# Kernel optimization log

Measured on AMD Instinct MI355X. Metric: run time of the kernel, lower is better.

## Reference

```python
import jax, jax.numpy as jnp
import numpy as np

# dims
BS = 4096
MOVE = 4
N_EN, ED = 64, 16
N_AL, AD = 63, 16
OTHER = 20
MF = MOVE + OTHER            # m_f_size = 24
IN = MOVE + N_EN * ED + N_AL * AD + OTHER  # 2056
H = 4                        # n_head
HE = 128                     # hypernet_emb
E = 64                       # attention_dim (emb_dim)
NA = N_EN + N_AL + 1         # n_agents = 128
RNN = 256
EN_START = MOVE
AL_START = MOVE + N_EN * ED
OTH_START = AL_START + N_AL * AD


def setup_inputs() -> dict:
    key = jax.random.key(0)
    ks = jax.random.split(key, 32)
    g = lambda k, shape: (jax.random.normal(k, shape, dtype=jnp.float32) * 0.05)
    return {
        "obs": jax.random.normal(ks[0], (BS, IN), dtype=jnp.float32),
        # per-head query MLP (Linear(MF,HE)+ReLU+Linear(HE,E,no bias)), stacked over heads
        "Wq1": g(ks[1], (H, HE, MF)), "bq1": g(ks[2], (H, HE)), "Wq2": g(ks[3], (H, E, HE)),
        # per-head key_m MLP
        "Wkm1": g(ks[4], (H, HE, MF)), "bkm1": g(ks[5], (H, HE)), "Wkm2": g(ks[6], (H, E, HE)),
        # per-head entity key linears (no bias)
        "Wke": g(ks[7], (H, E, ED)), "Wka": g(ks[8], (H, E, AD)),
        # per-head value_m MLP
        "Wvm1": g(ks[9], (H, HE, MF)), "bvm1": g(ks[10], (H, HE)), "Wvm2": g(ks[11], (H, E, HE)),
        # per-head entity value linears (no bias)
        "Wve": g(ks[12], (H, E, ED)), "Wva": g(ks[13], (H, E, AD)),
        # b net: Linear(IN,E)+ReLU+Linear(E,1)
        "Wb1": g(ks[14], (E, IN)), "bb1": g(ks[15], (E,)), "Wb2": g(ks[16], (1, E)), "bb2": g(ks[17], (1,)),
        # hyper_w_head: Linear(IN,HE)+ReLU+Linear(HE,H)
        "Wh1": g(ks[18], (HE, IN)), "bh1": g(ks[19], (HE,)), "Wh2": g(ks[20], (H, HE)), "bh2": g(ks[21], (H,)),
        # final layer: Linear(E*NA, RNN)
        "Wf": g(ks[22], (RNN, E * NA)), "bf": g(ks[23], (RNN,)),
    }


def _headed_mlp(x, W1, b1, W2):
    # x: [B, MF]; W1: [H, HE, MF]; W2: [H, E, HE] -> [B, H, E]
    h = jax.nn.relu(jnp.einsum("bf,hgf->bhg", x, W1) + b1[None])
    return jnp.einsum("bhg,heg->bhe", h, W2)


def reference(obs, Wq1, bq1, Wq2, Wkm1, bkm1, Wkm2, Wke, Wka,
              Wvm1, bvm1, Wvm2, Wve, Wva, Wb1, bb1, Wb2, bb2,
              Wh1, bh1, Wh2, bh2, Wf, bf):
    bs = obs.shape[0]
    m = jnp.concatenate([obs[:, :MOVE], obs[:, OTH_START:]], axis=1)        # [B, MF]
    enemies = obs[:, EN_START:AL_START].reshape(bs, N_EN, ED)               # [B, N_EN, ED]
    allies = obs[:, AL_START:OTH_START].reshape(bs, N_AL, AD)               # [B, N_AL, AD]

    q = _headed_mlp(m, Wq1, bq1, Wq2)                                       # [B, H, E]
    km = _headed_mlp(m, Wkm1, bkm1, Wkm2)[:, :, None, :]                    # [B, H, 1, E]
    ke = jnp.einsum("bnd,hed->bhne", enemies, Wke)                          # [B, H, N_EN, E]
    ka = jnp.einsum("bnd,hed->bhne", allies, Wka)                           # [B, H, N_AL, E]
    k = jnp.concatenate([km, ke, ka], axis=2)                               # [B, H, NA, E]

    vm = _headed_mlp(m, Wvm1, bvm1, Wvm2)[:, :, None, :]
    ve = jnp.einsum("bnd,hed->bhne", enemies, Wve)
    va = jnp.einsum("bnd,hed->bhne", allies, Wva)
    v = jnp.concatenate([vm, ve, va], axis=2)                               # [B, H, NA, E]

    logits = jnp.einsum("bhe,bhne->bhn", q, k) / np.sqrt(E).astype(np.float32)
    w = jax.nn.softmax(logits, axis=-1)                                     # [B, H, NA]
    # torch: atten_w (B,1,NA) expanded to (B,E,NA) * v permuted to (B,E,NA); flatten [E,NA]
    scores = (w[:, :, None, :] * jnp.swapaxes(v, 2, 3)).reshape(bs, H, E * NA)

    b_term = jax.nn.relu(obs @ Wb1.T + bb1) @ Wb2.T + bb2                   # [B, 1]
    w_head = jnp.abs(jax.nn.relu(obs @ Wh1.T + bh1) @ Wh2.T + bh2)          # [B, H]
    mixed = jnp.einsum("bhk,bh->bk", scores, w_head) + b_term               # [B, E*NA]
    return mixed @ Wf.T + bf                                                # [B, RNN]
```

## Files before the change

kernel.cpp:

```cpp
#include <hip/hip_runtime.h>
#include <hip/hip_bf16.h>

typedef __attribute__((ext_vector_type(8))) short short8;
typedef __attribute__((ext_vector_type(4))) float floatx4;

#define NIN 2056
#define KPAD 2080
#define NBS 4096

__device__ __forceinline__ void gl_lds16(const ushort* g, ushort* l) {
#if defined(__has_builtin) && __has_builtin(__builtin_amdgcn_global_load_lds)
  __builtin_amdgcn_global_load_lds(
      (const __attribute__((address_space(1))) unsigned int*)g,
      (__attribute__((address_space(3))) unsigned int*)l, 16, 0, 0);
#else
  *(uint4*)l = *(const uint4*)g;
#endif
}

__device__ __forceinline__ float wsum(float v) {
#pragma unroll
  for (int o = 32; o; o >>= 1) v += __shfl_xor(v, o, 64);
  return v;
}
__device__ __forceinline__ float wmax(float v) {
#pragma unroll
  for (int o = 32; o; o >>= 1) v = fmaxf(v, __shfl_xor(v, o, 64));
  return v;
}

__global__ void prep_small(const float* __restrict__ obs,
                           const float* __restrict__ Wb1, const float* __restrict__ Wh1,
                           const float* __restrict__ Wq1, const float* __restrict__ Wkm1,
                           const float* __restrict__ Wvm1, const float* __restrict__ bq1,
                           const float* __restrict__ bkm1, const float* __restrict__ bvm1,
                           const float* __restrict__ Wq2, const float* __restrict__ Wkm2,
                           const float* __restrict__ Wvm2,
                           const float* __restrict__ Wke, const float* __restrict__ Wka,
                           __hip_bfloat16* __restrict__ mmat,
                           __hip_bfloat16* __restrict__ w1cat,
                           __hip_bfloat16* __restrict__ w1m, float* __restrict__ b1cat,
                           __hip_bfloat16* __restrict__ w2cat,
                           __hip_bfloat16* __restrict__ wket,
                           __hip_bfloat16* __restrict__ wkat) {
  int bid = blockIdx.x, tid = threadIdx.x;
  if (bid < 512) {
    int idx = bid * 256 + tid;
    int b = idx >> 5, j = idx & 31;
    float v = 0.f;
    if (j < 4) v = obs[(size_t)b * NIN + j];
    else if (j < 24) v = obs[(size_t)b * NIN + 2032 + j];
    mmat[idx] = __float2bfloat16(v);
  } else if (bid < 704) {
    int r = bid - 512;
    const float* src = (r < 64) ? (Wb1 + (size_t)r * NIN) : (Wh1 + (size_t)(r - 64) * NIN);
    for (int j = tid; j < KPAD; j += 256)
      w1cat[(size_t)r * KPAD + j] = __float2bfloat16(j < NIN ? src[j] : 0.f);
  } else if (bid < 896) {
    int idx = (bid - 704) * 256 + tid;
    int row = idx >> 5, j = idx & 31;
    int net = row >> 9, hg = row & 511;
    const float* W1 = net == 0 ? Wq1 : (net == 1 ? Wkm1 : Wvm1);
    float v = (j < 24) ? W1[(size_t)hg * 24 + j] : 0.f;
    w1m[idx] = __float2bfloat16(v);
    if (j == 0) {
      const float* b1 = net == 0 ? bq1 : (net == 1 ? bkm1 : bvm1);
      b1cat[row] = b1[hg];
    }
  } else if (bid < 1280) {
    int idx = (bid - 896) * 256 + tid;
    int row = idx >> 7, g = idx & 127;
    int net = row >> 8, he = row & 255;
    const float* W2 = net == 0 ? Wq2 : (net == 1 ? Wkm2 : Wvm2);
    w2cat[idx] = __float2bfloat16(W2[(size_t)he * 128 + g]);
  } else {
    const float* W = (bid == 1280) ? Wke : Wka;
    __hip_bfloat16* dst = (bid == 1280) ? wket : wkat;
    for (int j = tid; j < 4096; j += 256) {
      int e = j & 63, hd = j >> 6;
      int h = hd >> 4, d = hd & 15;
      dst[j] = __float2bfloat16(W[h * 1024 + e * 16 + d]);
    }
  }
}

__global__ void p6a_twf(const float* __restrict__ Wf, float* __restrict__ Wft,
                        float* __restrict__ rowsum) {
  __shared__ float t[64][65];
  int kt = blockIdx.x, rt = blockIdx.y;
  int tid = threadIdx.x;
  int kl = tid & 63, r0 = tid >> 6;
#pragma unroll
  for (int ii = 0; ii < 16; ++ii) {
    int rl = ii * 4 + r0;
    t[rl][kl] = Wf[(size_t)(rt * 64 + rl) * 8192 + kt * 64 + kl];
  }
  __syncthreads();
#pragma unroll
  for (int ii = 0; ii < 16; ++ii) {
    int kl2 = ii * 4 + r0;
    Wft[(size_t)(kt * 64 + kl2) * 256 + rt * 64 + kl] = t[kl][kl2];
  }
  if (tid < 64) {
    float s = 0.f;
    for (int kk = 0; kk < 64; ++kk) s += t[tid][kk];
    atomicAdd(&rowsum[rt * 64 + tid], s);
  }
}

__global__ void p6b_yt(const float* __restrict__ Wft, const float* __restrict__ Wve,
                       const float* __restrict__ Wva, __hip_bfloat16* __restrict__ Yt) {
  int n = blockIdx.x;
  int r = threadIdx.x;
  if (n == 0) {
    alignas(16) __hip_bfloat16 tmp[8];
    for (int e0 = 0; e0 < 64; e0 += 8) {
#pragma unroll
      for (int j = 0; j < 8; ++j)
        tmp[j] = __float2bfloat16(Wft[(size_t)((e0 + j) * 128) * 256 + r]);
      *(uint4*)(Yt + (size_t)r * 8192 + (e0 >> 4) * 2048 + 2032 + (e0 & 15)) =
          *(const uint4*)tmp;
    }
    return;
  }
  const float* Wv = (n <= 64) ? Wve : Wva;
  float accv[64];
#pragma unroll
  for (int j = 0; j < 64; ++j) accv[j] = 0.f;
  for (int e = 0; e < 64; ++e) {
    float v = Wft[(size_t)(e * 128 + n) * 256 + r];
#pragma unroll
    for (int hd = 0; hd < 64; ++hd)
      accv[hd] += Wv[(hd >> 4) * 1024 + e * 16 + (hd & 15)] * v;
  }
#pragma unroll
  for (int c = 0; c < 8; ++c) {
    alignas(16) __hip_bfloat16 tmp[8];
#pragma unroll
    for (int j = 0; j < 8; ++j) tmp[j] = __float2bfloat16(accv[c * 8 + j]);
    *(uint4*)(Yt + (size_t)r * 8192 + (c >> 1) * 2048 + (size_t)(n - 1) * 16 + (c & 1) * 8) =
        *(const uint4*)tmp;
  }
}

__global__ __launch_bounds__(256) void qkv_fused(
    const __hip_bfloat16* __restrict__ mmat_, const __hip_bfloat16* __restrict__ w1m_,
    const float* __restrict__ b1cat, const __hip_bfloat16* __restrict__ w2cat_,
    const __hip_bfloat16* __restrict__ wket_, const __hip_bfloat16* __restrict__ wkat_,
    float* __restrict__ QKV, float* __restrict__ QKE, float* __restrict__ QKA) {
  __shared__ alignas(16) ushort lH[64 * 136];
  __shared__ alignas(16) ushort lq[64 * 72];
  const ushort* mmat = (const ushort*)mmat_;
  const ushort* w1m = (const ushort*)w1m_;
  const ushort* w2cat = (const ushort*)w2cat_;
  const ushort* wket = (const ushort*)wket_;
  const ushort* wkat = (const ushort*)wkat_;
  int mt = blockIdx.x, z = blockIdx.y;
  int t = threadIdx.x;
  int w = t >> 6, l = t & 63, r16 = l & 15, kg = l >> 4;
  floatx4 zero4 = {0.f, 0.f, 0.f, 0.f};
  short8 a1 = *(const short8*)(mmat + (size_t)(mt * 64 + w * 16 + r16) * 32 + kg * 8);
  floatx4 acc1[8];
#pragma unroll
  for (int c = 0; c < 8; ++c) {
    short8 b1 = *(const short8*)(w1m + (size_t)(z * 128 + c * 16 + r16) * 32 + kg * 8);
    acc1[c] = __builtin_amdgcn_mfma_f32_16x16x32_bf16(a1, b1, zero4, 0, 0, 0);
  }
#pragma unroll
  for (int c = 0; c < 8; ++c) {
    int col = c * 16 + r16;
    float bias = b1cat[z * 128 + col];
#pragma unroll
    for (int r = 0; r < 4; ++r) {
      float v = acc1[c][r] + bias;
      v = v > 0.f ? v : 0.f;
      __hip_bfloat16 bv = __float2bfloat16(v);
      lH[(w * 16 + kg * 4 + r) * 136 + col] = *(ushort*)&bv;
    }
  }
  __syncthreads();
  floatx4 acc2[4] = {zero4, zero4, zero4, zero4};
#pragma unroll
  for (int ks = 0; ks < 4; ++ks) {
    short8 a = *(const short8*)(lH + (w * 16 + r16) * 136 + ks * 32 + kg * 8);
#pragma unroll
    for (int c = 0; c < 4; ++c) {
      short8 b = *(const short8*)(w2cat + (size_t)(z * 64 + c * 16 + r16) * 128 + ks * 32 + kg * 8);
      acc2[c] = __builtin_amdgcn_mfma_f32_16x16x32_bf16(a, b, acc2[c], 0, 0, 0);
    }
  }
  float* Q = QKV + (size_t)(mt * 64) * 768 + z * 64;
#pragma unroll
  for (int c = 0; c < 4; ++c)
#pragma unroll
    for (int r = 0; r < 4; ++r)
      Q[(size_t)(w * 16 + kg * 4 + r) * 768 + c * 16 + r16] = acc2[c][r];
  if (z < 4) {
#pragma unroll
    for (int c = 0; c < 4; ++c)
#pragma unroll
      for (int r = 0; r < 4; ++r) {
        __hip_bfloat16 bv = __float2bfloat16(acc2[c][r]);
        lq[(w * 16 + kg * 4 + r) * 72 + c * 16 + r16] = *(ushort*)&bv;
      }
    short8 a0 = *(const short8*)(lq + (w * 16 + r16) * 72 + kg * 8);
    short8 a1q = *(const short8*)(lq + (w * 16 + r16) * 72 + 32 + kg * 8);
    const ushort* bke = wket + (size_t)(z * 16 + r16) * 64 + kg * 8;
    const ushort* bka = wkat + (size_t)(z * 16 + r16) * 64 + kg * 8;
    short8 bk0 = *(const short8*)bke;
    short8 bk1 = *(const short8*)(bke + 32);
    short8 ba0 = *(const short8*)bka;
    short8 ba1 = *(const short8*)(bka + 32);
    floatx4 ke = __builtin_amdgcn_mfma_f32_16x16x32_bf16(a0, bk0, zero4, 0, 0, 0);
    ke = __builtin_amdgcn_mfma_f32_16x16x32_bf16(a1q, bk1, ke, 0, 0, 0);
    floatx4 ka = __builtin_amdgcn_mfma_f32_16x16x32_bf16(a0, ba0, zero4, 0, 0, 0);
    ka = __builtin_amdgcn_mfma_f32_16x16x32_bf16(a1q, ba1, ka, 0, 0, 0);
#pragma unroll
    for (int r = 0; r < 4; ++r) {
      size_t row = (size_t)(mt * 64 + w * 16 + kg * 4 + r);
      QKE[row * 64 + z * 16 + r16] = ke[r];
      QKA[row * 64 + z * 16 + r16] = ka[r];
    }
  }
}

__global__ __launch_bounds__(256) void gemm_h1(
    const float* __restrict__ obs, const __hip_bfloat16* __restrict__ w1cat_,
    float* __restrict__ H1p) {
  __shared__ alignas(16) ushort lA[64 * 40];
  __shared__ alignas(16) ushort lB[192 * 40];
  const ushort* w1cat = (const ushort*)w1cat_;
  int mt = blockIdx.x, z = blockIdx.y;
  int t = threadIdx.x;
  int w = t >> 6, l = t & 63, r16 = l & 15, kg = l >> 4;
  int srow = t >> 2, sc = (t & 3) * 8;
  int k0 = z * 256;
  const float* ga = obs + (size_t)(mt * 64 + srow) * NIN + k0 + sc;
  ushort* sa = lA + srow * 40 + sc;
  const ushort* fa = lA + (w * 16 + r16) * 40 + kg * 8;
  floatx4 zero4 = {0.f, 0.f, 0.f, 0.f};
  floatx4 acc[12];
#pragma unroll
  for (int c = 0; c < 12; ++c) acc[c] = zero4;
  int nK = (z == 7) ? 9 : 8;
  for (int ks = 0; ks < nK; ++ks) {
    float4 f0, f1;
    bool tail = (z == 7 && ks == 8);
    if (!tail || (t & 3) == 0) {
      f0 = *(const float4*)(ga + ks * 32);
      f1 = *(const float4*)(ga + ks * 32 + 4);
    } else {
      f0 = make_float4(0.f, 0.f, 0.f, 0.f);
      f1 = make_float4(0.f, 0.f, 0.f, 0.f);
    }
    uint4 vb[3];
#pragma unroll
    for (int i = 0; i < 3; ++i)
      vb[i] = *(const uint4*)(w1cat + (size_t)(i * 64 + srow) * KPAD + k0 + sc + ks * 32);
    __syncthreads();
    alignas(16) __hip_bfloat16 tmp[8];
    tmp[0] = __float2bfloat16(f0.x); tmp[1] = __float2bfloat16(f0.y);
    tmp[2] = __float2bfloat16(f0.z); tmp[3] = __float2bfloat16(f0.w);
    tmp[4] = __float2bfloat16(f1.x); tmp[5] = __float2bfloat16(f1.y);
    tmp[6] = __float2bfloat16(f1.z); tmp[7] = __float2bfloat16(f1.w);
    *(uint4*)sa = *(const uint4*)tmp;
#pragma unroll
    for (int i = 0; i < 3; ++i)
      *(uint4*)(lB + (i * 64 + srow) * 40 + sc) = vb[i];
    __syncthreads();
    short8 a = *(const short8*)fa;
#pragma unroll
    for (int c = 0; c < 12; ++c) {
      short8 bb = *(const short8*)(lB + (c * 16 + r16) * 40 + kg * 8);
      acc[c] = __builtin_amdgcn_mfma_f32_16x16x32_bf16(a, bb, acc[c], 0, 0, 0);
    }
  }
  float* C = H1p + (size_t)z * NBS * 192;
  int row0 = mt * 64 + w * 16 + kg * 4;
#pragma unroll
  for (int c = 0; c < 12; ++c)
#pragma unroll
    for (int r = 0; r < 4; ++r)
      C[(size_t)(row0 + r) * 192 + c * 16 + r16] = acc[c][r];
}

__global__ __launch_bounds__(256) void gemm_final(
    const ushort* __restrict__ Xg, const ushort* __restrict__ Yt,
    float* __restrict__ part) {
  __shared__ alignas(16) ushort lA[128 * 32];
  __shared__ alignas(16) ushort lB[128 * 32];
  int bid = blockIdx.x;
  int z = bid & 7, nt = (bid >> 3) & 1, mt = bid >> 4;
  int t = threadIdx.x;
  int w = t >> 6, l = t & 63, r16 = l & 15, kg = l >> 4;
  int wr = (w >> 1) * 64, wc = (w & 1) * 64;
  const ushort* ga0 = Xg + (size_t)(mt * 128 + (t >> 2)) * 8192 + z * 1024 + (t & 3) * 8;
  const ushort* ga1 = ga0 + (size_t)64 * 8192;
  const ushort* gb0 = Yt + (size_t)(nt * 128 + (t >> 2)) * 8192 + z * 1024 + (t & 3) * 8;
  const ushort* gb1 = gb0 + (size_t)64 * 8192;
  ushort* la0 = lA + t * 8;
  ushort* la1 = lA + 2048 + t * 8;
  ushort* lb0 = lB + t * 8;
  ushort* lb1 = lB + 2048 + t * 8;
  const ushort* fa0 = lA + (wr + r16) * 32 + kg * 8;
  const ushort* fb0 = lB + (wc + r16) * 32 + kg * 8;
  floatx4 zero4 = {0.f, 0.f, 0.f, 0.f};
  floatx4 acc[4][4];
#pragma unroll
  for (int i = 0; i < 4; ++i)
#pragma unroll
    for (int j = 0; j < 4; ++j) acc[i][j] = zero4;
  for (int ks = 0; ks < 32; ++ks) {
    gl_lds16(ga0, la0);
    gl_lds16(ga1, la1);
    gl_lds16(gb0, lb0);
    gl_lds16(gb1, lb1);
    ga0 += 32; ga1 += 32; gb0 += 32; gb1 += 32;
    __syncthreads();
    short8 a[4], b[4];
#pragma unroll
    for (int mi = 0; mi < 4; ++mi) a[mi] = *(const short8*)(fa0 + mi * 512);
#pragma unroll
    for (int ni = 0; ni < 4; ++ni) b[ni] = *(const short8*)(fb0 + ni * 512);
#pragma unroll
    for (int mi = 0; mi < 4; ++mi)
#pragma unroll
      for (int ni = 0; ni < 4; ++ni)
        acc[mi][ni] = __builtin_amdgcn_mfma_f32_16x16x32_bf16(a[mi], b[ni], acc[mi][ni], 0, 0, 0);
    __syncthreads();
  }
  int row0 = mt * 128 + wr + kg * 4;
  int col0 = nt * 128 + wc + r16;
  float* cp = part + (size_t)z * NBS * 256;
#pragma unroll
  for (int mi = 0; mi < 4; ++mi)
#pragma unroll
    for (int ni = 0; ni < 4; ++ni)
#pragma unroll
      for (int r = 0; r < 4; ++r)
        cp[(size_t)(row0 + mi * 16 + r) * 256 + col0 + ni * 16] = acc[mi][ni][r];
}

__global__ __launch_bounds__(256) void row_kernel(
    const float* __restrict__ obs, const float* __restrict__ QKV,
    const float* __restrict__ QKE, const float* __restrict__ QKA,
    const float* __restrict__ H1p, const float* __restrict__ Wb2,
    const float* __restrict__ bb2, const float* __restrict__ Wh2,
    const float* __restrict__ bh2, const float* __restrict__ bb1,
    const float* __restrict__ bh1, __hip_bfloat16* __restrict__ X,
    float* __restrict__ bterm) {
  __shared__ float qke_lds[4][64], qka_lds[4][64];
  __shared__ uint4 xstage[4][2][256];
  int wv = threadIdx.x >> 6;
  int lane = threadIdx.x & 63;
  int b = blockIdx.x * 4 + wv;
  qke_lds[wv][lane] = QKE[(size_t)b * 64 + lane];
  qka_lds[wv][lane] = QKA[(size_t)b * 64 + lane];
  const float* qkv = QKV + (size_t)b * 768;
  float q_h[4], km_h[4], vm_h[4];
#pragma unroll
  for (int h = 0; h < 4; ++h) {
    q_h[h] = qkv[h * 64 + lane];
    km_h[h] = qkv[256 + h * 64 + lane];
    vm_h[h] = qkv[512 + h * 64 + lane];
  }
  float l0[4];
#pragma unroll
  for (int h = 0; h < 4; ++h) l0[h] = wsum(q_h[h] * km_h[h]) * 0.125f;
  const float* ob = obs + (size_t)b * NIN;
  alignas(16) float en[16];
  alignas(16) float al[16];
  {
    const float4* ep = (const float4*)(ob + 4 + lane * 16);
    const float4* ap = (const float4*)(ob + 1028 + lane * 16);
#pragma unroll
    for (int i = 0; i < 4; ++i) {
      *(float4*)(en + 4 * i) = ep[i];
      *(float4*)(al + 4 * i) = ap[i];
    }
  }
  bool av = lane < 63;
  float lE[4], lA_[4];
#pragma unroll
  for (int h = 0; h < 4; ++h) {
    float sE = 0.f, sA = 0.f;
#pragma unroll
    for (int d = 0; d < 16; ++d) {
      sE += en[d] * qke_lds[wv][h * 16 + d];
      sA += al[d] * qka_lds[wv][h * 16 + d];
    }
    lE[h] = sE * 0.125f;
    lA_[h] = sA * 0.125f;
  }
  float vb0 = 0.f, vw0 = 0.f, vw1 = 0.f;
  const size_t S1 = (size_t)NBS * 192;
#pragma unroll
  for (int z = 0; z < 8; ++z) {
    const float* p = H1p + (size_t)z * S1 + (size_t)b * 192;
    vb0 += p[lane];
    vw0 += p[64 + lane];
    vw1 += p[128 + lane];
  }
  float hb = fmaxf(vb0 + bb1[lane], 0.f);
  float bt = wsum(hb * Wb2[lane]) + bb2[0];
  float hw0 = fmaxf(vw0 + bh1[lane], 0.f);
  float hw1 = fmaxf(vw1 + bh1[64 + lane], 0.f);
  float whead[4];
#pragma unroll
  for (int h = 0; h < 4; ++h)
    whead[h] = fabsf(wsum(hw0 * Wh2[h * 128 + lane] + hw1 * Wh2[h * 128 + 64 + lane]) + bh2[h]);
  float wE[4], wA[4], w0[4];
#pragma unroll
  for (int h = 0; h < 4; ++h) {
    float mE = wmax(lE[h]);
    float mA = wmax(av ? lA_[h] : -3.0e38f);
    float mx = fmaxf(fmaxf(mE, mA), l0[h]);
    float pE = __expf(lE[h] - mx);
    float pA = av ? __expf(lA_[h] - mx) : 0.f;
    float p0 = __expf(l0[h] - mx);
    float den = wsum(pE + pA) + p0;
    float s = whead[h] / den;
    wE[h] = pE * s;
    wA[h] = pA * s;
    w0[h] = p0 * s;
  }
  __hip_bfloat16* xr = X + (size_t)b * 8192;
#pragma unroll
  for (int h = 0; h < 4; ++h) {
    int buf = h & 1;
    uint ue[8], ua[8];
#pragma unroll
    for (int j = 0; j < 8; ++j) {
      __hip_bfloat16 lo = __float2bfloat16(wE[h] * en[2 * j]);
      __hip_bfloat16 hi = __float2bfloat16(wE[h] * en[2 * j + 1]);
      ue[j] = (uint)*(ushort*)&lo | ((uint)*(ushort*)&hi << 16);
      __hip_bfloat16 alo = __float2bfloat16(wA[h] * al[2 * j]);
      __hip_bfloat16 ahi = __float2bfloat16(wA[h] * al[2 * j + 1]);
      ua[j] = (uint)*(ushort*)&alo | ((uint)*(ushort*)&ahi << 16);
    }
    xstage[wv][buf][lane * 2] = make_uint4(ue[0], ue[1], ue[2], ue[3]);
    xstage[wv][buf][lane * 2 + 1] = make_uint4(ue[4], ue[5], ue[6], ue[7]);
    if (av) {
      xstage[wv][buf][(64 + lane) * 2] = make_uint4(ua[0], ua[1], ua[2], ua[3]);
      xstage[wv][buf][(64 + lane) * 2 + 1] = make_uint4(ua[4], ua[5], ua[6], ua[7]);
    }
#pragma unroll
    for (int s = 0; s < 4; ++s) {
      uint4 v = xstage[wv][buf][s * 64 + lane];
      if (!(s == 3 && lane >= 62))
        *(uint4*)(xr + h * 2048 + s * 512 + lane * 8) = v;
    }
  }
  float x0 = w0[0] * vm_h[0] + w0[1] * vm_h[1] + w0[2] * vm_h[2] + w0[3] * vm_h[3];
  xr[(lane >> 4) * 2048 + 2032 + (lane & 15)] = __float2bfloat16(x0);
  if (lane == 0) bterm[b] = bt;
}

__global__ void k7_out(const float* __restrict__ part, const float* __restrict__ bterm,
                       const float* __restrict__ rowsum, const float* __restrict__ bfv,
                       float* __restrict__ out) {
  int b = blockIdx.x, r = threadIdx.x;
  size_t i = (size_t)b * 256 + r;
  const size_t S = (size_t)NBS * 256;
  float v = 0.f;
#pragma unroll
  for (int z = 0; z < 8; ++z) v += part[i + z * S];
  out[i] = v + bterm[b] * rowsum[r] + bfv[r];
}

extern "C" void kernel_launch(void* const* d_in, const int* in_sizes, int n_in,
                              void* d_out, int out_size, void* d_ws, size_t ws_size,
                              hipStream_t stream) {
  const float* obs = (const float*)d_in[0];
  const float* Wq1 = (const float*)d_in[1];
  const float* bq1 = (const float*)d_in[2];
  const float* Wq2 = (const float*)d_in[3];
  const float* Wkm1 = (const float*)d_in[4];
  const float* bkm1 = (const float*)d_in[5];
  const float* Wkm2 = (const float*)d_in[6];
  const float* Wke = (const float*)d_in[7];
  const float* Wka = (const float*)d_in[8];
  const float* Wvm1 = (const float*)d_in[9];
  const float* bvm1 = (const float*)d_in[10];
  const float* Wvm2 = (const float*)d_in[11];
  const float* Wve = (const float*)d_in[12];
  const float* Wva = (const float*)d_in[13];
  const float* Wb1 = (const float*)d_in[14];
  const float* bb1 = (const float*)d_in[15];
  const float* Wb2 = (const float*)d_in[16];
  const float* bb2 = (const float*)d_in[17];
  const float* Wh1 = (const float*)d_in[18];
  const float* bh1 = (const float*)d_in[19];
  const float* Wh2 = (const float*)d_in[20];
  const float* bh2 = (const float*)d_in[21];
  const float* Wf = (const float*)d_in[22];
  const float* bfv = (const float*)d_in[23];
  float* out = (float*)d_out;

  char* ws = (char*)d_ws;
  size_t off = 0;
  auto alloc = [&](size_t bytes) -> void* {
    void* p = ws + off;
    off += (bytes + 255) & ~(size_t)255;
    return p;
  };
  __hip_bfloat16* mmat = (__hip_bfloat16*)alloc((size_t)NBS * 32 * 2);
  __hip_bfloat16* w1m = (__hip_bfloat16*)alloc((size_t)1536 * 32 * 2);
  float* b1cat = (float*)alloc(1536 * 4);
  __hip_bfloat16* w2cat = (__hip_bfloat16*)alloc((size_t)768 * 128 * 2);
  __hip_bfloat16* w1cat = (__hip_bfloat16*)alloc((size_t)192 * KPAD * 2);
  __hip_bfloat16* wket = (__hip_bfloat16*)alloc(4096 * 2);
  __hip_bfloat16* wkat = (__hip_bfloat16*)alloc(4096 * 2);
  float* rowsum = (float*)alloc(256 * 4);
  float* bterm = (float*)alloc(NBS * 4);
  float* QKE = (float*)alloc((size_t)NBS * 64 * 4);
  float* QKA = (float*)alloc((size_t)NBS * 64 * 4);
  float* Wft = (float*)alloc((size_t)8192 * 256 * 4);
  __hip_bfloat16* Yt = (__hip_bfloat16*)alloc((size_t)256 * 8192 * 2);
  __hip_bfloat16* X = (__hip_bfloat16*)alloc((size_t)NBS * 8192 * 2);
  char* R = (char*)alloc((size_t)39 * 1024 * 1024);
  float* QKV = (float*)R;
  float* H1p = (float*)(R + (size_t)NBS * 768 * 4);
  float* part8 = (float*)R;

  hipMemsetAsync(rowsum, 0, 256 * 4, stream);

  prep_small<<<1282, 256, 0, stream>>>(obs, Wb1, Wh1, Wq1, Wkm1, Wvm1, bq1, bkm1, bvm1,
                                       Wq2, Wkm2, Wvm2, Wke, Wka,
                                       mmat, w1cat, w1m, b1cat, w2cat, wket, wkat);
  p6a_twf<<<dim3(128, 4), 256, 0, stream>>>(Wf, Wft, rowsum);
  p6b_yt<<<128, 256, 0, stream>>>(Wft, Wve, Wva, Yt);

  gemm_h1<<<dim3(64, 8), 256, 0, stream>>>(obs, w1cat, H1p);
  qkv_fused<<<dim3(64, 12), 256, 0, stream>>>(mmat, w1m, b1cat, w2cat, wket, wkat,
                                              QKV, QKE, QKA);
  row_kernel<<<NBS / 4, 256, 0, stream>>>(obs, QKV, QKE, QKA, H1p, Wb2, bb2, Wh2, bh2,
                                          bb1, bh1, X, bterm);
  gemm_final<<<512, 256, 0, stream>>>((const ushort*)X, (const ushort*)Yt, part8);
  k7_out<<<NBS, 256, 0, stream>>>(part8, bterm, rowsum, bfv, out);

  (void)in_sizes; (void)n_in; (void)out_size; (void)ws_size;
}
```

Before: 264.2 us.

## Split gemm_h1 over N tiles and prefetch next K-slice into registers

The gemm_h1 kernel now adds an N grid dimension (3 tiles of 64 columns), so each block computes a 64x64 output tile instead of 64x192. This triples the block count and cuts accumulator and LDS use per block. It also moves the global loads for the next K step after the barrier, so they overlap with the MFMA work on the current step. In exchange, each obs tile is read and converted three times.

```diff
diff --git a/kernel.cpp b/kernel.cpp
--- a/kernel.cpp
+++ b/kernel.cpp
@@ -228,60 +228,66 @@
     const float* __restrict__ obs, const __hip_bfloat16* __restrict__ w1cat_,
     float* __restrict__ H1p) {
   __shared__ alignas(16) ushort lA[64 * 40];
-  __shared__ alignas(16) ushort lB[192 * 40];
+  __shared__ alignas(16) ushort lB[64 * 40];
   const ushort* w1cat = (const ushort*)w1cat_;
-  int mt = blockIdx.x, z = blockIdx.y;
+  int mt = blockIdx.x, nt = blockIdx.y, z = blockIdx.z;
   int t = threadIdx.x;
   int w = t >> 6, l = t & 63, r16 = l & 15, kg = l >> 4;
   int srow = t >> 2, sc = (t & 3) * 8;
   int k0 = z * 256;
   const float* ga = obs + (size_t)(mt * 64 + srow) * NIN + k0 + sc;
+  const ushort* gb = w1cat + (size_t)(nt * 64 + srow) * KPAD + k0 + sc;
   ushort* sa = lA + srow * 40 + sc;
+  ushort* sb = lB + srow * 40 + sc;
   const ushort* fa = lA + (w * 16 + r16) * 40 + kg * 8;
+  const ushort* fb0 = lB + r16 * 40 + kg * 8;
   floatx4 zero4 = {0.f, 0.f, 0.f, 0.f};
-  floatx4 acc[12];
-#pragma unroll
-  for (int c = 0; c < 12; ++c) acc[c] = zero4;
+  floatx4 acc[4] = {zero4, zero4, zero4, zero4};
   int nK = (z == 7) ? 9 : 8;
+  bool aok = (t & 3) == 0;
+  float4 f0c, f1c;
+  uint4 vbc;
+  {
+    f0c = *(const float4*)(ga);
+    f1c = *(const float4*)(ga + 4);
+    vbc = *(const uint4*)(gb);
+  }
   for (int ks = 0; ks < nK; ++ks) {
-    float4 f0, f1;
-    bool tail = (z == 7 && ks == 8);
-    if (!tail || (t & 3) == 0) {
-      f0 = *(const float4*)(ga + ks * 32);
-      f1 = *(const float4*)(ga + ks * 32 + 4);
-    } else {
-      f0 = make_float4(0.f, 0.f, 0.f, 0.f);
-      f1 = make_float4(0.f, 0.f, 0.f, 0.f);
-    }
-    uint4 vb[3];
-#pragma unroll
-    for (int i = 0; i < 3; ++i)
-      vb[i] = *(const uint4*)(w1cat + (size_t)(i * 64 + srow) * KPAD + k0 + sc + ks * 32);
     __syncthreads();
     alignas(16) __hip_bfloat16 tmp[8];
-    tmp[0] = __float2bfloat16(f0.x); tmp[1] = __float2bfloat16(f0.y);
-    tmp[2] = __float2bfloat16(f0.z); tmp[3] = __float2bfloat16(f0.w);
-    tmp[4] = __float2bfloat16(f1.x); tmp[5] = __float2bfloat16(f1.y);
-    tmp[6] = __float2bfloat16(f1.z); tmp[7] = __float2bfloat16(f1.w);
+    tmp[0] = __float2bfloat16(f0c.x); tmp[1] = __float2bfloat16(f0c.y);
+    tmp[2] = __float2bfloat16(f0c.z); tmp[3] = __float2bfloat16(f0c.w);
+    tmp[4] = __float2bfloat16(f1c.x); tmp[5] = __float2bfloat16(f1c.y);
+    tmp[6] = __float2bfloat16(f1c.z); tmp[7] = __float2bfloat16(f1c.w);
     *(uint4*)sa = *(const uint4*)tmp;
-#pragma unroll
-    for (int i = 0; i < 3; ++i)
-      *(uint4*)(lB + (i * 64 + srow) * 40 + sc) = vb[i];
+    *(uint4*)sb = vbc;
     __syncthreads();
+    if (ks + 1 < nK) {
+      bool tail = (z == 7 && ks + 1 == 8);
+      if (!tail || aok) {
+        f0c = *(const float4*)(ga + (ks + 1) * 32);
+        f1c = *(const float4*)(ga + (ks + 1) * 32 + 4);
+      } else {
+        f0c = make_float4(0.f, 0.f, 0.f, 0.f);
+        f1c = make_float4(0.f, 0.f, 0.f, 0.f);
+      }
+      vbc = *(const uint4*)(gb + (ks + 1) * 32);
+    }
     short8 a = *(const short8*)fa;
 #pragma unroll
-    for (int c = 0; c < 12; ++c) {
-      short8 bb = *(const short8*)(lB + (c * 16 + r16) * 40 + kg * 8);
+    for (int c = 0; c < 4; ++c) {
+      short8 bb = *(const short8*)(fb0 + c * 16 * 40);
       acc[c] = __builtin_amdgcn_mfma_f32_16x16x32_bf16(a, bb, acc[c], 0, 0, 0);
     }
   }
   float* C = H1p + (size_t)z * NBS * 192;
   int row0 = mt * 64 + w * 16 + kg * 4;
-#pragma unroll
-  for (int c = 0; c < 12; ++c)
+  int col0 = nt * 64 + r16;
+#pragma unroll
+  for (int c = 0; c < 4; ++c)
 #pragma unroll
     for (int r = 0; r < 4; ++r)
-      C[(size_t)(row0 + r) * 192 + c * 16 + r16] = acc[c][r];
+      C[(size_t)(row0 + r) * 192 + col0 + c * 16] = acc[c][r];
 }
 
 __global__ __launch_bounds__(256) void gemm_final(
@@ -531,7 +537,7 @@
   p6a_twf<<<dim3(128, 4), 256, 0, stream>>>(Wf, Wft, rowsum);
   p6b_yt<<<128, 256, 0, stream>>>(Wft, Wve, Wva, Yt);
 
-  gemm_h1<<<dim3(64, 8), 256, 0, stream>>>(obs, w1cat, H1p);
+  gemm_h1<<<dim3(64, 3, 8), 256, 0, stream>>>(obs, w1cat, H1p);
   qkv_fused<<<dim3(64, 12), 256, 0, stream>>>(mmat, w1m, b1cat, w2cat, wket, wkat,
                                               QKV, QKE, QKA);
   row_kernel<<<NBS / 4, 256, 0, stream>>>(obs, QKV, QKE, QKA, H1p, Wb2, bb2, Wh2, bh2,
```

Measured after the change: 251.8 us. 1.05x faster.
